# Optimization experiments

Hardware: AMD Instinct MI355X
Metric: run time of the kernel (lower is better)

The kernel has to match this reference:

```python
import jax, jax.numpy as jnp
import numpy as np

EPS = 1e-5

def _bn(x, w, b, rm, rv):
    # eval-mode BatchNorm over channel axis (x: [..., C] broadcastable)
    return (x - rm) * (w * jax.lax.rsqrt(rv + EPS)) + b

def setup_inputs() -> dict:
    key = jax.random.key(0)
    ks = jax.random.split(key, 20)
    B, C, H, W = 2, 64, 96, 96
    Cq = C // 8  # query/key channels
    Cr = C // 8  # SE reduction channels
    s = 0.05
    inp = {
        'x': jax.random.normal(ks[0], (B, C, H, W), jnp.float32),
        'wq': jax.random.normal(ks[1], (Cq, C), jnp.float32) * s,
        'bq': jnp.zeros((Cq,), jnp.float32),
        'wk': jax.random.normal(ks[2], (Cq, C), jnp.float32) * s,
        'bk': jnp.zeros((Cq,), jnp.float32),
        'wv': jax.random.normal(ks[3], (C, C), jnp.float32) * s,
        'bv': jnp.zeros((C,), jnp.float32),
        'gamma': jnp.full((1,), 0.5, jnp.float32),
        'bn_w': jnp.ones((C,), jnp.float32),
        'bn_b': jnp.zeros((C,), jnp.float32),
        'bn_rm': jax.random.normal(ks[4], (C,), jnp.float32) * 0.1,
        'bn_rv': jax.random.uniform(ks[5], (C,), jnp.float32) + 0.5,
        'se_w1': jax.random.normal(ks[6], (Cr, C), jnp.float32) * s,
        'se_b1': jnp.zeros((Cr,), jnp.float32),
        'se_bn1_w': jnp.ones((Cr,), jnp.float32),
        'se_bn1_b': jnp.zeros((Cr,), jnp.float32),
        'se_bn1_rm': jax.random.normal(ks[7], (Cr,), jnp.float32) * 0.1,
        'se_bn1_rv': jax.random.uniform(ks[8], (Cr,), jnp.float32) + 0.5,
        'se_w2': jax.random.normal(ks[9], (C, Cr), jnp.float32) * s,
        'se_b2': jnp.zeros((C,), jnp.float32),
        'se_bn2_w': jnp.ones((C,), jnp.float32),
        'se_bn2_b': jnp.zeros((C,), jnp.float32),
        'se_bn2_rm': jax.random.normal(ks[10], (C,), jnp.float32) * 0.1,
        'se_bn2_rv': jax.random.uniform(ks[11], (C,), jnp.float32) + 0.5,
    }
    return inp

def reference(x, wq, bq, wk, bk, wv, bv, gamma, bn_w, bn_b, bn_rm, bn_rv,
              se_w1, se_b1, se_bn1_w, se_bn1_b, se_bn1_rm, se_bn1_rv,
              se_w2, se_b2, se_bn2_w, se_bn2_b, se_bn2_rm, se_bn2_rv):
    B, C, H, W = x.shape
    N = H * W
    xf = x.reshape(B, C, N)
    # PAM branch: 1x1 conv projections
    q = jnp.einsum('oc,bcn->bno', wq, xf) + bq            # [B,N,C/8]
    k = jnp.einsum('oc,bcn->bon', wk, xf) + bk[:, None]    # [B,C/8,N]
    v = jnp.einsum('oc,bcn->bon', wv, xf) + bv[:, None]    # [B,C,N]
    energy = jnp.einsum('bno,bom->bnm', q, k)              # [B,N,N]
    attn = jax.nn.softmax(energy, axis=-1)
    # out[b,c,i] = sum_j v[b,c,j] * attn[b,i,j]  (bmm(V, attn^T))
    out = jnp.einsum('bcj,bij->bci', v, attn)
    out = gamma[0] * out
    out = _bn(out, bn_w[:, None], bn_b[:, None], bn_rm[:, None], bn_rv[:, None])
    pam = out.reshape(B, C, H, W)
    # SE branch: GAP + 1x1 conv-bn-relu x2, multiplicative gate
    a = xf.mean(axis=2)                                    # [B,C]
    a1 = jax.nn.relu(_bn(a @ se_w1.T + se_b1, se_bn1_w, se_bn1_b, se_bn1_rm, se_bn1_rv))
    a2 = jax.nn.relu(_bn(a1 @ se_w2.T + se_b2, se_bn2_w, se_bn2_b, se_bn2_rm, se_bn2_rv))
    se = x * a2[:, :, None, None]
    return x + se + pam
```

## Files before the change

### kernel.cpp

```cpp
#include <hip/hip_runtime.h>
#include <hip/hip_bf16.h>

#define B_SZ   2
#define C_CH   64
#define NQ     8
#define QKS    16
#define NPIX   9216
#define NKS    576
#define QBLKS  288
#define KPART  4
#define NSPLIT 4
#define KEYS_W 576
#define SM_F   2080
#define PSLOT  2080
#define NP4    2304
#define KSTEP2 1024
#define VSTEP  4096

typedef short bf16x8 __attribute__((ext_vector_type(8)));
typedef float f32x4  __attribute__((ext_vector_type(4)));
typedef float f32x16 __attribute__((ext_vector_type(16)));
typedef unsigned u32x4 __attribute__((ext_vector_type(4)));
typedef unsigned uint2v __attribute__((ext_vector_type(2)));

static __device__ __forceinline__ unsigned pack2bf(float a, float b){
    unsigned r;
    asm("v_cvt_pk_bf16_f32 %0, %1, %2" : "=v"(r) : "v"(a), "v"(b));
    return r;
}

static __device__ __forceinline__ float exp2r(float x){
    return __builtin_amdgcn_exp2f(x);
}

__global__ __launch_bounds__(256) void prep_kernel(
    const float* __restrict__ x,
    const float* __restrict__ wq, const float* __restrict__ bq,
    const float* __restrict__ wk, const float* __restrict__ bk,
    const float* __restrict__ wv, const float* __restrict__ bv,
    __hip_bfloat16* __restrict__ qp, __hip_bfloat16* __restrict__ kp,
    __hip_bfloat16* __restrict__ vswz, float* __restrict__ amean)
{
    const int blk = blockIdx.x, tid = threadIdx.x;
    if (blk < 144){
        int t  = blk*256 + tid;
        int n  = (t % NP4) * 4;
        int c8 = (t / NP4) & 7;
        int b  = t / (NP4*8);
        c8 = __builtin_amdgcn_readfirstlane(c8);
        b  = __builtin_amdgcn_readfirstlane(b);
        float acc[8][4];
#pragma unroll
        for (int k = 0; k < 8; ++k){
            float bvv = bv[c8*8 + k];
            acc[k][0] = bvv; acc[k][1] = bvv; acc[k][2] = bvv; acc[k][3] = bvv;
        }
#pragma unroll 4
        for (int ci = 0; ci < C_CH; ++ci){
            const float4 xv = *reinterpret_cast<const float4*>(
                x + (size_t)(b*C_CH + ci)*NPIX + n);
#pragma unroll
            for (int k = 0; k < 8; ++k){
                float w = wv[(c8*8 + k)*C_CH + ci];
                acc[k][0] = fmaf(xv.x, w, acc[k][0]);
                acc[k][1] = fmaf(xv.y, w, acc[k][1]);
                acc[k][2] = fmaf(xv.z, w, acc[k][2]);
                acc[k][3] = fmaf(xv.w, w, acc[k][3]);
            }
        }
#pragma unroll
        for (int k = 0; k < 8; ++k){
            int c = c8*8 + k;
            size_t base = ((size_t)((b*NKS + (n >> 4))*2 + (c >> 5)))*512
                        + (((n >> 3) & 1) << 8) + ((c & 31) << 3) + (n & 7);
            unsigned long long wpk =
                (unsigned long long)pack2bf(acc[k][0], acc[k][1]) |
                ((unsigned long long)pack2bf(acc[k][2], acc[k][3]) << 32);
            *reinterpret_cast<unsigned long long*>(vswz + base) = wpk;
        }
    } else if (blk < 180){
        int t  = (blk - 144)*256 + tid;
        int n  = (t % NP4) * 4;
        int o8 = (t / NP4) & 1;
        int b  = t / (NP4*2);
        o8 = __builtin_amdgcn_readfirstlane(o8);
        b  = __builtin_amdgcn_readfirstlane(b);
        const bool isq = (o8 == 0);
        const float* w    = isq ? wq : wk;
        const float* bias = isq ? bq : bk;
        float acc[8][4];
#pragma unroll
        for (int k = 0; k < 8; ++k){
            float bb = bias[k];
            acc[k][0] = bb; acc[k][1] = bb; acc[k][2] = bb; acc[k][3] = bb;
        }
#pragma unroll 4
        for (int ci = 0; ci < C_CH; ++ci){
            const float4 xv = *reinterpret_cast<const float4*>(
                x + (size_t)(b*C_CH + ci)*NPIX + n);
#pragma unroll
            for (int k = 0; k < 8; ++k){
                float wv_ = w[k*C_CH + ci];
                acc[k][0] = fmaf(xv.x, wv_, acc[k][0]);
                acc[k][1] = fmaf(xv.y, wv_, acc[k][1]);
                acc[k][2] = fmaf(xv.z, wv_, acc[k][2]);
                acc[k][3] = fmaf(xv.w, wv_, acc[k][3]);
            }
        }
        if (isq){
#pragma unroll
            for (int k = 0; k < 8; ++k)
#pragma unroll
                for (int px = 0; px < 4; ++px) acc[k][px] *= 1.44269504f;
        }
        __hip_bfloat16* dst = isq ? qp : kp;
        u32x4 zr; zr[0] = 0; zr[1] = 0; zr[2] = 0; zr[3] = 0;
#pragma unroll
        for (int px = 0; px < 4; ++px){
            u32x4 row;
            row[0] = pack2bf(acc[0][px], acc[1][px]);
            row[1] = pack2bf(acc[2][px], acc[3][px]);
            row[2] = pack2bf(acc[4][px], acc[5][px]);
            row[3] = pack2bf(acc[6][px], acc[7][px]);
            __hip_bfloat16* d0 = dst + ((size_t)(b*NPIX + n + px))*QKS;
            *reinterpret_cast<u32x4*>(d0)     = row;
            *reinterpret_cast<u32x4*>(d0 + 8) = zr;
        }
    } else {
        int bc = blk - 180;
        float s = 0.f;
        for (int i = tid; i < NPIX; i += 256) s += x[(size_t)bc*NPIX + i];
#pragma unroll
        for (int o = 32; o > 0; o >>= 1) s += __shfl_down(s, o, 64);
        __shared__ float red[4];
        if ((tid & 63) == 0) red[tid >> 6] = s;
        __syncthreads();
        if (tid == 0) amean[bc] = (red[0] + red[1] + red[2] + red[3]) * (1.f / (float)NPIX);
    }
}

__global__ __launch_bounds__(256) void flash_fused(
    const __hip_bfloat16* __restrict__ qp,
    const __hip_bfloat16* __restrict__ kp,
    const __hip_bfloat16* __restrict__ vswz,
    float* __restrict__ pws)
{
    __shared__ __align__(16) float sm[2*SM_F];

    const int qt2 = blockIdx.x, b = blockIdx.y, z = blockIdx.z;
    const int p  = threadIdx.x >> 6;
    const int l  = threadIdx.x & 63;
    const int lc = l & 31;
    const int lh = l >> 5;

    bf16x8 qfrag = *reinterpret_cast<const bf16x8*>(
        qp + ((size_t)(b*NPIX + qt2*32 + lc))*QKS + lh*8);

    bf16x8 ones;
#pragma unroll
    for (int i = 0; i < 8; ++i) ones[i] = (short)0x3F80;

    f32x16 zero16;
#pragma unroll
    for (int i = 0; i < 16; ++i) zero16[i] = 0.f;

    f32x16 Of0 = zero16, Of1 = zero16;
    f32x16 Lacc = zero16;

    const int kpart = z*KPART + p;
    const __hip_bfloat16* kptr = kp + ((size_t)(b*NPIX + kpart*KEYS_W + lc))*QKS + lh*8;
    const __hip_bfloat16* vptr = vswz + ((size_t)((b*NKS + kpart*(KEYS_W/16))*2))*512 + l*8;

    auto CHUNK = [&](const bf16x8& k0, const bf16x8& k1){
        const __hip_bfloat16* vA = vptr;
        const __hip_bfloat16* vB = vptr + 4*512;
        bf16x8 vf[8];
#pragma unroll
        for (int t = 0; t < 4; ++t)
            vf[t] = *reinterpret_cast<const bf16x8*>(vA + t*512);
#pragma unroll
        for (int t = 0; t < 4; ++t)
            vf[4+t] = *reinterpret_cast<const bf16x8*>(vB + t*512);
        vptr += VSTEP;

        unsigned D[16];
#pragma unroll
        for (int kt = 0; kt < 2; ++kt){
            f32x16 s = __builtin_amdgcn_mfma_f32_32x32x16_bf16(
                kt ? k1 : k0, qfrag, zero16, 0, 0, 0);
#pragma unroll
            for (int g = 0; g < 4; ++g){
                float e0 = exp2r(s[4*g+0]), e1 = exp2r(s[4*g+1]);
                float e2 = exp2r(s[4*g+2]), e3 = exp2r(s[4*g+3]);
                D[kt*8 + g*2 + 0] = pack2bf(e0, e1);
                D[kt*8 + g*2 + 1] = pack2bf(e2, e3);
            }
        }
        __builtin_amdgcn_s_setprio(1);
#pragma unroll
        for (int ks = 0; ks < 4; ++ks){
            const int base = (ks >> 1)*8 + (ks & 1)*4;
            uint2v r0 = __builtin_amdgcn_permlane32_swap(D[base+0], D[base+2], false, false);
            uint2v r1 = __builtin_amdgcn_permlane32_swap(D[base+1], D[base+3], false, false);
            u32x4 pu; pu[0] = r0[0]; pu[1] = r1[0]; pu[2] = r0[1]; pu[3] = r1[1];
            bf16x8 pf = __builtin_bit_cast(bf16x8, pu);
            Of0  = __builtin_amdgcn_mfma_f32_32x32x16_bf16(vf[ks*2+0], pf, Of0, 0, 0, 0);
            Of1  = __builtin_amdgcn_mfma_f32_32x32x16_bf16(vf[ks*2+1], pf, Of1, 0, 0, 0);
            Lacc = __builtin_amdgcn_mfma_f32_32x32x16_bf16(ones,       pf, Lacc, 0, 0, 0);
        }
        __builtin_amdgcn_s_setprio(0);
    };

    bf16x8 kA0, kA1, kB0, kB1;
    kA0 = *reinterpret_cast<const bf16x8*>(kptr);
    kA1 = *reinterpret_cast<const bf16x8*>(kptr + 512);
    kptr += KSTEP2;
    for (int it = 0; it < 4; ++it){
        kB0 = *reinterpret_cast<const bf16x8*>(kptr);
        kB1 = *reinterpret_cast<const bf16x8*>(kptr + 512);
        kptr += KSTEP2;
        CHUNK(kA0, kA1);
        kA0 = *reinterpret_cast<const bf16x8*>(kptr);
        kA1 = *reinterpret_cast<const bf16x8*>(kptr + 512);
        if (it < 3) kptr += KSTEP2;
        CHUNK(kB0, kB1);
    }
    CHUNK(kA0, kA1);

    if (p >= 2){
        const int ps = p - 2;
#pragma unroll
        for (int r = 0; r < 16; ++r){
            sm[ps*SM_F +        r*64 + l] = Of0[r];
            sm[ps*SM_F + 1024 + r*64 + l] = Of1[r];
        }
        if (l < 32) sm[ps*SM_F + 2048 + l] = Lacc[0];
    }
    __syncthreads();
    if (p < 2){
#pragma unroll
        for (int r = 0; r < 16; ++r){
            sm[p*SM_F +        r*64 + l] += Of0[r];
            sm[p*SM_F + 1024 + r*64 + l] += Of1[r];
        }
        if (l < 32) sm[p*SM_F + 2048 + l] += Lacc[0];
    }
    __syncthreads();

    {
        float* dst = pws + ((size_t)((b*QBLKS + qt2)*NSPLIT + z))*PSLOT;
        for (int i = threadIdx.x; i < PSLOT; i += 256)
            dst[i] = sm[i] + sm[SM_F + i];
    }
}

__global__ __launch_bounds__(256) void combine_kernel(
    const float* __restrict__ pws,
    const float* __restrict__ amean,
    const float* __restrict__ sw1, const float* __restrict__ sb1,
    const float* __restrict__ s1w, const float* __restrict__ s1b,
    const float* __restrict__ s1m, const float* __restrict__ s1v,
    const float* __restrict__ sw2, const float* __restrict__ sb2,
    const float* __restrict__ s2w, const float* __restrict__ s2b,
    const float* __restrict__ s2m, const float* __restrict__ s2v,
    const float* __restrict__ x,
    const float* __restrict__ gamma,
    const float* __restrict__ bnw, const float* __restrict__ bnb,
    const float* __restrict__ bnm, const float* __restrict__ bnv,
    float* __restrict__ out)
{
    const int qt2 = blockIdx.x, b = blockIdx.y;
    const int p  = threadIdx.x >> 6;
    const int l  = threadIdx.x & 63;
    const int lc = l & 31;
    const int lh = l >> 5;

    float a1r;
    {
        int r8 = l & 7;
        float s = sb1[r8];
#pragma unroll 8
        for (int c = 0; c < C_CH; ++c)
            s = fmaf(amean[b*C_CH + c], sw1[r8*C_CH + c], s);
        s = (s - s1m[r8]) * (s1w[r8] * rsqrtf(s1v[r8] + 1e-5f)) + s1b[r8];
        a1r = fmaxf(s, 0.f);
    }

    const float* P0 = pws + ((size_t)((b*QBLKS + qt2)*NSPLIT))*PSLOT;

    const int i   = lc;
    const int cgs = p*2 + lh;
    float gam = gamma[0];

    float a1g[8];
#pragma unroll
    for (int j = 0; j < 8; ++j) a1g[j] = __shfl(a1r, (l & 56) | j, 64);

    float L = 0.f;
#pragma unroll
    for (int zz = 0; zz < NSPLIT; ++zz) L += P0[zz*PSLOT + 2048 + i];
    float invL = 1.f / L;
    int n = qt2*32 + i;
#pragma unroll
    for (int r = 0; r < 8; ++r){
        int c = cgs*8 + r;
        float s = sb2[c];
#pragma unroll
        for (int j = 0; j < 8; ++j) s = fmaf(a1g[j], sw2[c*NQ + j], s);
        s = (s - s2m[c]) * (s2w[c] * rsqrtf(s2v[c] + 1e-5f)) + s2b[c];
        float a2v = fmaxf(s, 0.f);

        int c5   = c & 31;
        int reg  = (c5 & 3) + 4*(c5 >> 3);
        int lsrc = (c5 >> 2) & 1;
        int o    = (c >> 5)*1024 + reg*64 + lsrc*32 + i;
        float O = 0.f;
#pragma unroll
        for (int zz = 0; zz < NSPLIT; ++zz) O += P0[zz*PSLOT + o];
        float pam = gam * O * invL;
        pam = (pam - bnm[c]) * (bnw[c] * rsqrtf(bnv[c] + 1e-5f)) + bnb[c];
        float xv = x[(size_t)(b*C_CH + c)*NPIX + n];
        out[(size_t)(b*C_CH + c)*NPIX + n] = fmaf(xv, a2v, xv + pam);
    }
}

extern "C" void kernel_launch(void* const* d_in, const int* in_sizes, int n_in,
                              void* d_out, int out_size, void* d_ws, size_t ws_size,
                              hipStream_t stream)
{
    const float* x     = (const float*)d_in[0];
    const float* wq    = (const float*)d_in[1];
    const float* bq    = (const float*)d_in[2];
    const float* wk    = (const float*)d_in[3];
    const float* bk    = (const float*)d_in[4];
    const float* wv    = (const float*)d_in[5];
    const float* bv    = (const float*)d_in[6];
    const float* gamma = (const float*)d_in[7];
    const float* bnw   = (const float*)d_in[8];
    const float* bnb   = (const float*)d_in[9];
    const float* bnm   = (const float*)d_in[10];
    const float* bnv   = (const float*)d_in[11];
    const float* sw1   = (const float*)d_in[12];
    const float* sb1   = (const float*)d_in[13];
    const float* s1w   = (const float*)d_in[14];
    const float* s1b   = (const float*)d_in[15];
    const float* s1m   = (const float*)d_in[16];
    const float* s1v   = (const float*)d_in[17];
    const float* sw2   = (const float*)d_in[18];
    const float* sb2   = (const float*)d_in[19];
    const float* s2w   = (const float*)d_in[20];
    const float* s2b   = (const float*)d_in[21];
    const float* s2m   = (const float*)d_in[22];
    const float* s2v   = (const float*)d_in[23];

    size_t off = 0;
    auto give = [&](size_t bytes) -> void* {
        void* r = (char*)d_ws + off;
        off += (bytes + 255) & ~(size_t)255;
        return r;
    };
    __hip_bfloat16* qp   = (__hip_bfloat16*)give((size_t)B_SZ*NPIX*QKS*2);
    __hip_bfloat16* kp   = (__hip_bfloat16*)give((size_t)B_SZ*NPIX*QKS*2);
    __hip_bfloat16* vswz = (__hip_bfloat16*)give((size_t)B_SZ*C_CH*NPIX*2);
    float* amean = (float*)give((size_t)B_SZ*C_CH*4);
    float* pws   = (float*)give((size_t)B_SZ*QBLKS*NSPLIT*PSLOT*4);

    prep_kernel<<<dim3(308), dim3(256), 0, stream>>>(x, wq, bq, wk, bk, wv, bv,
                                                     qp, kp, vswz, amean);
    flash_fused<<<dim3(QBLKS, B_SZ, NSPLIT), dim3(256), 0, stream>>>(qp, kp, vswz, pws);
    combine_kernel<<<dim3(QBLKS, B_SZ), dim3(256), 0, stream>>>(
        pws, amean,
        sw1, sb1, s1w, s1b, s1m, s1v,
        sw2, sb2, s2w, s2b, s2m, s2v,
        x, gamma, bnw, bnb, bnm, bnv, (float*)d_out);
}
```

Measured before the change: 175.8 us.

## Fuse Q/K/V projections into one LDS-tiled block per pixel tile

Measured after the change: 175.0 us. About the same (-0.4%).

```diff
diff --git a/kernel.cpp b/kernel.cpp
--- a/kernel.cpp
+++ b/kernel.cpp
@@ -13,9 +13,9 @@
 #define KEYS_W 576
 #define SM_F   2080
 #define PSLOT  2080
-#define NP4    2304
 #define KSTEP2 1024
 #define VSTEP  4096
+#define PTILES 72
 
 typedef short bf16x8 __attribute__((ext_vector_type(8)));
 typedef float f32x4  __attribute__((ext_vector_type(4)));
@@ -43,91 +43,94 @@
 {
     const int blk = blockIdx.x, tid = threadIdx.x;
     if (blk < 144){
-        int t  = blk*256 + tid;
-        int n  = (t % NP4) * 4;
-        int c8 = (t / NP4) & 7;
-        int b  = t / (NP4*8);
-        c8 = __builtin_amdgcn_readfirstlane(c8);
-        b  = __builtin_amdgcn_readfirstlane(b);
-        float acc[8][4];
-#pragma unroll
-        for (int k = 0; k < 8; ++k){
-            float bvv = bv[c8*8 + k];
-            acc[k][0] = bvv; acc[k][1] = bvv; acc[k][2] = bvv; acc[k][3] = bvv;
+        __shared__ float xs[64*128];
+        __shared__ float ws[80*65];
+        const int b  = blk / PTILES;
+        const int n0 = (blk % PTILES) * 128;
+
+        for (int i = tid; i < 80*64; i += 256){
+            int r = i >> 6, ci = i & 63;
+            float v = (r < 64) ? wv[r*64 + ci]
+                    : (r < 72) ? wq[(r-64)*64 + ci]
+                               : wk[(r-72)*64 + ci];
+            ws[r*65 + ci] = v;
+        }
+        float4* xs4 = reinterpret_cast<float4*>(xs);
+        for (int i = tid; i < 2048; i += 256){
+            int ci = i >> 5, p4 = i & 31;
+            xs4[i] = *reinterpret_cast<const float4*>(
+                x + (size_t)(b*C_CH + ci)*NPIX + n0 + p4*4);
+        }
+        __syncthreads();
+
+        const int og = tid >> 4;
+        const int po = tid & 15;
+        float acc[5][8];
+#pragma unroll
+        for (int oi = 0; oi < 5; ++oi){
+            int o = og*5 + oi;
+            float bb = (o < 64) ? bv[o] : (o < 72) ? bq[o-64] : bk[o-72];
+#pragma unroll
+            for (int px = 0; px < 8; ++px) acc[oi][px] = bb;
         }
 #pragma unroll 4
         for (int ci = 0; ci < C_CH; ++ci){
-            const float4 xv = *reinterpret_cast<const float4*>(
-                x + (size_t)(b*C_CH + ci)*NPIX + n);
-#pragma unroll
-            for (int k = 0; k < 8; ++k){
-                float w = wv[(c8*8 + k)*C_CH + ci];
-                acc[k][0] = fmaf(xv.x, w, acc[k][0]);
-                acc[k][1] = fmaf(xv.y, w, acc[k][1]);
-                acc[k][2] = fmaf(xv.z, w, acc[k][2]);
-                acc[k][3] = fmaf(xv.w, w, acc[k][3]);
+            float4 xa = xs4[ci*32 + po*2];
+            float4 xb = xs4[ci*32 + po*2 + 1];
+#pragma unroll
+            for (int oi = 0; oi < 5; ++oi){
+                float w = ws[(og*5 + oi)*65 + ci];
+                acc[oi][0] = fmaf(xa.x, w, acc[oi][0]);
+                acc[oi][1] = fmaf(xa.y, w, acc[oi][1]);
+                acc[oi][2] = fmaf(xa.z, w, acc[oi][2]);
+                acc[oi][3] = fmaf(xa.w, w, acc[oi][3]);
+                acc[oi][4] = fmaf(xb.x, w, acc[oi][4]);
+                acc[oi][5] = fmaf(xb.y, w, acc[oi][5]);
+                acc[oi][6] = fmaf(xb.z, w, acc[oi][6]);
+                acc[oi][7] = fmaf(xb.w, w, acc[oi][7]);
             }
         }
 #pragma unroll
-        for (int k = 0; k < 8; ++k){
-            int c = c8*8 + k;
-            size_t base = ((size_t)((b*NKS + (n >> 4))*2 + (c >> 5)))*512
-                        + (((n >> 3) & 1) << 8) + ((c & 31) << 3) + (n & 7);
-            unsigned long long wpk =
-                (unsigned long long)pack2bf(acc[k][0], acc[k][1]) |
-                ((unsigned long long)pack2bf(acc[k][2], acc[k][3]) << 32);
-            *reinterpret_cast<unsigned long long*>(vswz + base) = wpk;
-        }
-    } else if (blk < 180){
-        int t  = (blk - 144)*256 + tid;
-        int n  = (t % NP4) * 4;
-        int o8 = (t / NP4) & 1;
-        int b  = t / (NP4*2);
-        o8 = __builtin_amdgcn_readfirstlane(o8);
-        b  = __builtin_amdgcn_readfirstlane(b);
-        const bool isq = (o8 == 0);
-        const float* w    = isq ? wq : wk;
-        const float* bias = isq ? bq : bk;
-        float acc[8][4];
-#pragma unroll
-        for (int k = 0; k < 8; ++k){
-            float bb = bias[k];
-            acc[k][0] = bb; acc[k][1] = bb; acc[k][2] = bb; acc[k][3] = bb;
-        }
-#pragma unroll 4
-        for (int ci = 0; ci < C_CH; ++ci){
-            const float4 xv = *reinterpret_cast<const float4*>(
-                x + (size_t)(b*C_CH + ci)*NPIX + n);
-#pragma unroll
-            for (int k = 0; k < 8; ++k){
-                float wv_ = w[k*C_CH + ci];
-                acc[k][0] = fmaf(xv.x, wv_, acc[k][0]);
-                acc[k][1] = fmaf(xv.y, wv_, acc[k][1]);
-                acc[k][2] = fmaf(xv.z, wv_, acc[k][2]);
-                acc[k][3] = fmaf(xv.w, wv_, acc[k][3]);
+        for (int oi = 0; oi < 5; ++oi){
+            int o = og*5 + oi;
+            if (o < 64){
+                int c = o;
+#pragma unroll
+                for (int qd = 0; qd < 2; ++qd){
+                    int n = n0 + po*8 + qd*4;
+                    size_t base = ((size_t)((b*NKS + (n >> 4))*2 + (c >> 5)))*512
+                                + (((n >> 3) & 1) << 8) + ((c & 31) << 3) + (n & 7);
+                    unsigned long long wpk =
+                        (unsigned long long)pack2bf(acc[oi][qd*4+0], acc[oi][qd*4+1]) |
+                        ((unsigned long long)pack2bf(acc[oi][qd*4+2], acc[oi][qd*4+3]) << 32);
+                    *reinterpret_cast<unsigned long long*>(vswz + base) = wpk;
+                }
+            } else if (o < 72){
+                int oq = o - 64;
+#pragma unroll
+                for (int px = 0; px < 8; ++px){
+                    int n = n0 + po*8 + px;
+                    unsigned u = pack2bf(acc[oi][px] * 1.44269504f, 0.f);
+                    unsigned short* d = reinterpret_cast<unsigned short*>(
+                        qp + ((size_t)(b*NPIX + n))*QKS);
+                    d[oq]     = (unsigned short)(u & 0xffff);
+                    d[8 + oq] = 0;
+                }
+            } else {
+                int ok = o - 72;
+#pragma unroll
+                for (int px = 0; px < 8; ++px){
+                    int n = n0 + po*8 + px;
+                    unsigned u = pack2bf(acc[oi][px], 0.f);
+                    unsigned short* d = reinterpret_cast<unsigned short*>(
+                        kp + ((size_t)(b*NPIX + n))*QKS);
+                    d[ok]     = (unsigned short)(u & 0xffff);
+                    d[8 + ok] = 0;
+                }
             }
         }
-        if (isq){
-#pragma unroll
-            for (int k = 0; k < 8; ++k)
-#pragma unroll
-                for (int px = 0; px < 4; ++px) acc[k][px] *= 1.44269504f;
-        }
-        __hip_bfloat16* dst = isq ? qp : kp;
-        u32x4 zr; zr[0] = 0; zr[1] = 0; zr[2] = 0; zr[3] = 0;
-#pragma unroll
-        for (int px = 0; px < 4; ++px){
-            u32x4 row;
-            row[0] = pack2bf(acc[0][px], acc[1][px]);
-            row[1] = pack2bf(acc[2][px], acc[3][px]);
-            row[2] = pack2bf(acc[4][px], acc[5][px]);
-            row[3] = pack2bf(acc[6][px], acc[7][px]);
-            __hip_bfloat16* d0 = dst + ((size_t)(b*NPIX + n + px))*QKS;
-            *reinterpret_cast<u32x4*>(d0)     = row;
-            *reinterpret_cast<u32x4*>(d0 + 8) = zr;
-        }
     } else {
-        int bc = blk - 180;
+        int bc = blk - 144;
         float s = 0.f;
         for (int i = tid; i < NPIX; i += 256) s += x[(size_t)bc*NPIX + i];
 #pragma unroll
@@ -365,7 +368,7 @@
     float* amean = (float*)give((size_t)B_SZ*C_CH*4);
     float* pws   = (float*)give((size_t)B_SZ*QBLKS*NSPLIT*PSLOT*4);
 
-    prep_kernel<<<dim3(308), dim3(256), 0, stream>>>(x, wq, bq, wk, bk, wv, bv,
+    prep_kernel<<<dim3(272), dim3(256), 0, stream>>>(x, wq, bq, wk, bk, wv, bv,
                                                      qp, kp, vswz, amean);
     flash_fused<<<dim3(QBLKS, B_SZ, NSPLIT), dim3(256), 0, stream>>>(qp, kp, vswz, pws);
     combine_kernel<<<dim3(QBLKS, B_SZ), dim3(256), 0, stream>>>(
```
